# Optimization experiments

Measured on AMD Instinct MI355X. Metric: run time of the kernel, lower is better.

The kernel has to match this reference:

```python
import jax, jax.numpy as jnp
import numpy as np
import math

N, LQ, DIM = 4, 1000, 256
HEADS, DHEAD, DEPTH = 8, 32, 2
LVLS, NPTS, MLP = 5, 4, 512
SCALE = DHEAD ** -0.5
SHAPES = np.array([[128, 128], [64, 64], [32, 32], [16, 16], [8, 8]], np.int32)
AREAS = SHAPES[:, 0] * SHAPES[:, 1]
STARTS = np.concatenate([[0], np.cumsum(AREAS)[:-1]]).astype(np.int32)
LIN = int(AREAS.sum())


def _ln(x, g, b):
    m = jnp.mean(x, -1, keepdims=True)
    v = jnp.var(x, -1, keepdims=True)
    return (x - m) * jax.lax.rsqrt(v + 1e-5) * g + b


def _gelu(x):  # tanh-approx GELU exactly as the torch module
    c = math.sqrt(2.0 / math.pi)
    return 0.5 * x * (1.0 + jnp.tanh(c * (x + 0.044715 * x ** 3)))


def _ms_deform(value, shapes, starts, loc, aw):
    # value [N,Lin,H,D]; loc [N,Lq,H,L,P,2] normalized to [0,1]; aw [N,Lq,H,L,P]
    n, lq, h, L, p, _ = loc.shape
    d = value.shape[-1]
    ni = jnp.arange(n)[:, None, None, None]
    hi = jnp.arange(h)[None, None, :, None]
    out = jnp.zeros((n, lq, h, d), value.dtype)
    for l in range(L):  # fixed small pyramid depth
        Hl, Wl = int(shapes[l, 0]), int(shapes[l, 1])
        s = int(starts[l])
        v = value[:, s:s + Hl * Wl].reshape(n, Hl, Wl, h, d)
        gx = loc[:, :, :, l, :, 0] * Wl - 0.5  # [N,Lq,H,P]
        gy = loc[:, :, :, l, :, 1] * Hl - 0.5
        x0 = jnp.floor(gx); y0 = jnp.floor(gy)
        lx = gx - x0; ly = gy - y0
        x0i = x0.astype(jnp.int32); y0i = y0.astype(jnp.int32)
        def corner(yi, xi):
            ok = ((yi >= 0) & (yi < Hl) & (xi >= 0) & (xi < Wl)).astype(value.dtype)
            g = v[ni, jnp.clip(yi, 0, Hl - 1), jnp.clip(xi, 0, Wl - 1), hi]  # [N,Lq,H,P,D]
            return g * ok[..., None]
        samp = (corner(y0i, x0i) * ((1 - ly) * (1 - lx))[..., None]
                + corner(y0i, x0i + 1) * ((1 - ly) * lx)[..., None]
                + corner(y0i + 1, x0i) * (ly * (1 - lx))[..., None]
                + corner(y0i + 1, x0i + 1) * (ly * lx)[..., None])
        out = out + jnp.einsum('nqhp,nqhpd->nqhd', aw[:, :, :, l], samp)
    return out.reshape(n, lq, h * d)


def _forward(x, src, center_pos, pos_w, pos_b, ln1_g, ln1_b, qkv_w, out_w, out_b,
             ln2_g, ln2_b, off_w, off_b, aw_w, aw_b, val_w, val_b, op_w, op_b,
             ln3_g, ln3_b, ff_w1, ff_b1, ff_w2, ff_b2, spatial_shapes, level_start_index):
    shapes = np.asarray(spatial_shapes)
    starts = np.asarray(level_start_index)
    n, lq, dim = x.shape
    pe = center_pos @ pos_w + pos_b                                   # pos_embedding(center_pos)
    ref = jnp.broadcast_to(center_pos[:, :, None, :], (n, lq, LVLS, 2))
    onorm = jnp.asarray(np.stack([shapes[:, 1], shapes[:, 0]], -1), x.dtype)  # [L,2] = (W,H)
    for i in range(DEPTH):
        # --- self-attention: PreNorm(x + pe) ---
        xn = _ln(x + pe, ln1_g[i], ln1_b[i])
        qkv = xn @ qkv_w[i]
        q, k, v = jnp.split(qkv, 3, axis=-1)
        q = q.reshape(n, lq, HEADS, DHEAD).transpose(0, 2, 1, 3)
        k = k.reshape(n, lq, HEADS, DHEAD).transpose(0, 2, 1, 3)
        v = v.reshape(n, lq, HEADS, DHEAD).transpose(0, 2, 1, 3)
        att = jax.nn.softmax(jnp.einsum('nhid,nhjd->nhij', q, k) * SCALE, axis=-1)
        o = jnp.einsum('nhij,nhjd->nhid', att, v).transpose(0, 2, 1, 3).reshape(n, lq, HEADS * DHEAD)
        x = x + o @ out_w[i] + out_b[i]
        # --- deformable cross-attention: PreNorm_CA norms query and src with same LN ---
        xn = _ln(x, ln2_g[i], ln2_b[i])
        srcn = _ln(src, ln2_g[i], ln2_b[i])
        query = xn + pe
        value = (srcn @ val_w[i] + val_b[i]).reshape(n, -1, HEADS, DHEAD)
        off = (query @ off_w[i] + off_b[i]).reshape(n, lq, HEADS, LVLS, NPTS, 2)
        aw = jax.nn.softmax((query @ aw_w[i] + aw_b[i]).reshape(n, lq, HEADS, LVLS * NPTS), axis=-1)
        aw = aw.reshape(n, lq, HEADS, LVLS, NPTS)
        loc = ref[:, :, None, :, None, :] + off / onorm[None, None, None, :, None, :]
        o = _ms_deform(value, shapes, starts, loc, aw)
        x = x + o @ op_w[i] + op_b[i]
        # --- feedforward: PreNorm ---
        xn = _ln(x, ln3_g[i], ln3_b[i])
        x = x + _gelu(xn @ ff_w1[i] + ff_b1[i]) @ ff_w2[i] + ff_b2[i]
    return x


def setup_inputs() -> dict:
    key = jax.random.key(0)
    ks = iter(jax.random.split(key, 64))
    r = lambda sh, s=0.02: jax.random.normal(next(ks), sh, jnp.float32) * s
    # sampling_offsets bias grid init (as in MSDeformAttn._reset_parameters)
    thetas = np.arange(HEADS) * (2.0 * math.pi / HEADS)
    grid = np.stack([np.cos(thetas), np.sin(thetas)], -1)
    grid = grid / np.abs(grid).max(-1, keepdims=True)
    grid = np.tile(grid[:, None, None, :], (1, LVLS, NPTS, 1)) * (np.arange(NPTS) + 1)[None, None, :, None]
    off_b = jnp.tile(jnp.asarray(grid.reshape(-1), jnp.float32)[None], (DEPTH, 1))
    return dict(
        x=jax.random.normal(next(ks), (N, LQ, DIM), jnp.float32),
        src=jax.random.normal(next(ks), (N, LIN, DIM), jnp.float32),
        center_pos=jax.random.uniform(next(ks), (N, LQ, 2), jnp.float32),
        spatial_shapes=jnp.asarray(SHAPES),
        level_start_index=jnp.asarray(STARTS),
        pos_w=r((2, DIM), 0.5), pos_b=jnp.zeros((DIM,), jnp.float32),
        ln1_g=jnp.ones((DEPTH, DIM), jnp.float32), ln1_b=jnp.zeros((DEPTH, DIM), jnp.float32),
        qkv_w=r((DEPTH, DIM, 3 * HEADS * DHEAD)),
        out_w=r((DEPTH, HEADS * DHEAD, DIM)), out_b=jnp.zeros((DEPTH, DIM), jnp.float32),
        ln2_g=jnp.ones((DEPTH, DIM), jnp.float32), ln2_b=jnp.zeros((DEPTH, DIM), jnp.float32),
        off_w=r((DEPTH, DIM, HEADS * LVLS * NPTS * 2)), off_b=off_b,
        aw_w=r((DEPTH, DIM, HEADS * LVLS * NPTS)), aw_b=jnp.zeros((DEPTH, HEADS * LVLS * NPTS), jnp.float32),
        val_w=r((DEPTH, DIM, HEADS * DHEAD)), val_b=jnp.zeros((DEPTH, HEADS * DHEAD), jnp.float32),
        op_w=r((DEPTH, HEADS * DHEAD, DIM)), op_b=jnp.zeros((DEPTH, DIM), jnp.float32),
        ln3_g=jnp.ones((DEPTH, DIM), jnp.float32), ln3_b=jnp.zeros((DEPTH, DIM), jnp.float32),
        ff_w1=r((DEPTH, DIM, MLP)), ff_b1=jnp.zeros((DEPTH, MLP), jnp.float32),
        ff_w2=r((DEPTH, MLP, DIM)), ff_b2=jnp.zeros((DEPTH, DIM), jnp.float32),
    )


def reference(x, src, center_pos, spatial_shapes, level_start_index, pos_w, pos_b,
              ln1_g, ln1_b, qkv_w, out_w, out_b, ln2_g, ln2_b, off_w, off_b,
              aw_w, aw_b, val_w, val_b, op_w, op_b, ln3_g, ln3_b,
              ff_w1, ff_b1, ff_w2, ff_b2):
    return _forward(x, src, center_pos, pos_w, pos_b, ln1_g, ln1_b, qkv_w, out_w, out_b,
                    ln2_g, ln2_b, off_w, off_b, aw_w, aw_b, val_w, val_b, op_w, op_b,
                    ln3_g, ln3_b, ff_w1, ff_b1, ff_w2, ff_b2, spatial_shapes, level_start_index)
```

## Files before the change

### kernel.cpp

```cpp
#include <hip/hip_runtime.h>
#include <hip/hip_bf16.h>
#include <math.h>

#define DIM 256
#define NB 4
#define LQ 1000
#define MLPD 512
#define LIN 21824
#define ROWS_X 4000
#define ROWS_SRC 87296
#define ATT_SCALE 0.17677669529663687f
#define LDK 72

typedef __hip_bfloat16 bf16;
typedef __attribute__((ext_vector_type(8))) short short8;
typedef __attribute__((ext_vector_type(4))) float floatx4;

__device__ __forceinline__ float rdv(const void* p, int f, size_t i){
    if (f) return ((const float*)p)[i];
    unsigned u = ((unsigned)((const unsigned short*)p)[i]) << 16;
    union { unsigned u; float f; } c; c.u = u; return c.f;
}
__device__ __forceinline__ short f2bs(float v){
    bf16 h = __float2bfloat16(v);
    return *reinterpret_cast<short*>(&h);
}
__device__ __forceinline__ float bs2f(short s){
    union { unsigned u; float f; } c; c.u = ((unsigned)(unsigned short)s) << 16; return c.f;
}

__global__ void detect_kernel(const void* __restrict__ x, int* __restrict__ flag){
    const unsigned short* u = (const unsigned short*)x;
    int t = threadIdx.x;
    bool hit = false;
    #pragma unroll
    for (int k = 0; k < 4; ++k) {
        unsigned short b = u[(t*4 + k)*2];
        union { unsigned u; float f; } c; c.u = ((unsigned)b) << 16;
        if (!(fabsf(c.f) <= 1000.f)) hit = true;
    }
    unsigned long long m = __ballot(hit);
    __shared__ unsigned long long red[4];
    if ((t & 63) == 0) red[t >> 6] = m;
    __syncthreads();
    if (t == 0) flag[0] = ((red[0]|red[1]|red[2]|red[3]) != 0ULL) ? 1 : 0;
}

__global__ void conv_kernel(const void* __restrict__ in, float* __restrict__ out,
                            int n, const int* __restrict__ flag){
    int f = flag[0];
    int i = blockIdx.x*256 + threadIdx.x;
    if (i < n) out[i] = rdv(in, f, i);
}

struct PTab { const void* src[14]; float* dst[14]; int n[14]; };
__global__ void convs_kernel(PTab t, const int* __restrict__ flag){
    int f = flag[0];
    int j = blockIdx.y;
    int i = blockIdx.x*256 + threadIdx.x;
    if (i < t.n[j]) t.dst[j][i] = rdv(t.src[j], f, i);
}

__global__ void catb_kernel(const void* __restrict__ offb, const void* __restrict__ awb,
                            const int* __restrict__ flag, float* __restrict__ oab){
    int f = flag[0];
    int layer = blockIdx.y;
    int idx = blockIdx.x*256 + threadIdx.x;
    if (idx >= 480) return;
    float v = (idx < 320) ? rdv(offb, f, (size_t)layer*320 + idx)
                          : rdv(awb,  f, (size_t)layer*160 + idx - 320);
    oab[layer*480 + idx] = v;
}

struct WT { const void* src[8]; short* dst[8]; int K[8]; int N[8]; int ld[8]; int ro[8]; };
__global__ void wtransall_kernel(WT t, const int* __restrict__ flag){
    int j = blockIdx.z >> 1, b = blockIdx.z & 1;
    int K = t.K[j], N = t.N[j];
    int k0 = blockIdx.x*32, n0 = blockIdx.y*32;
    if (k0 >= K || n0 >= N) return;
    int f = flag[0];
    __shared__ float tt[32][33];
    int tx = threadIdx.x & 31, ty = threadIdx.x >> 5;
    size_t base = (size_t)b * K * N;
    for (int i = ty; i < 32; i += 8) {
        int k = k0 + i, n = n0 + tx;
        tt[i][tx] = (k < K && n < N) ? rdv(t.src[j], f, base + (size_t)k*N + n) : 0.f;
    }
    __syncthreads();
    int ld = t.ld[j], ro = t.ro[j];
    for (int i = ty; i < 32; i += 8) {
        int n = n0 + i, k = k0 + tx;
        if (n < N && k < K)
            t.dst[j][(size_t)b*ld*K + (size_t)(ro+n)*K + k] = f2bs(tt[tx][i]);
    }
}

__global__ void pe_kernel(const void* __restrict__ cp, const void* __restrict__ pw,
                          const void* __restrict__ pb, const int* __restrict__ flag,
                          float* __restrict__ pe){
    int f = flag[0];
    int row = blockIdx.x, t = threadIdx.x;
    float cx = rdv(cp, f, (size_t)row*2);
    float cy = rdv(cp, f, (size_t)row*2 + 1);
    pe[(size_t)row*DIM + t] = cx*rdv(pw, f, t) + cy*rdv(pw, f, DIM + t) + rdv(pb, f, t);
}

__global__ __launch_bounds__(256) void stats2_kernel(const void* __restrict__ src,
                                                     const int* __restrict__ flag,
                                                     float2* __restrict__ stats){
    int f = flag[0];
    int wave = threadIdx.x >> 6, lane = threadIdx.x & 63;
    int row = blockIdx.x*4 + wave;
    float v0, v1, v2, v3;
    if (f) {
        float4 x = *(const float4*)((const float*)src + (size_t)row*DIM + lane*4);
        v0 = x.x; v1 = x.y; v2 = x.z; v3 = x.w;
    } else {
        ushort4 u = *(const ushort4*)((const unsigned short*)src + (size_t)row*DIM + lane*4);
        v0 = bs2f((short)u.x); v1 = bs2f((short)u.y);
        v2 = bs2f((short)u.z); v3 = bs2f((short)u.w);
    }
    float s  = v0 + v1 + v2 + v3;
    float s2 = v0*v0 + v1*v1 + v2*v2 + v3*v3;
    #pragma unroll
    for (int o = 32; o; o >>= 1) {
        s  += __shfl_xor(s,  o, 64);
        s2 += __shfl_xor(s2, o, 64);
    }
    if (lane == 0) {
        float mean = s * (1.f/DIM);
        float var  = s2 * (1.f/DIM) - mean*mean;
        stats[row] = make_float2(mean, rsqrtf(var + 1e-5f));
    }
}

__global__ __launch_bounds__(256) void xstats_kernel(const float* __restrict__ a,
                                                     const float* __restrict__ pre,
                                                     float2* __restrict__ st){
    int wave = threadIdx.x >> 6, lane = threadIdx.x & 63;
    int row = blockIdx.x*4 + wave;
    float4 x = *(const float4*)(a + (size_t)row*DIM + lane*4);
    if (pre) {
        float4 p = *(const float4*)(pre + (size_t)row*DIM + lane*4);
        x.x += p.x; x.y += p.y; x.z += p.z; x.w += p.w;
    }
    float s  = x.x + x.y + x.z + x.w;
    float s2 = x.x*x.x + x.y*x.y + x.z*x.z + x.w*x.w;
    #pragma unroll
    for (int o = 32; o; o >>= 1) {
        s  += __shfl_xor(s,  o, 64);
        s2 += __shfl_xor(s2, o, 64);
    }
    if (lane == 0) {
        float mean = s * (1.f/DIM);
        float var  = s2 * (1.f/DIM) - mean*mean;
        st[row] = make_float2(mean, rsqrtf(var + 1e-5f));
    }
}

template<int AMODE>
__global__ __launch_bounds__(256) void mgemm_kernel(
    const void* __restrict__ Asrc,
    const float2* __restrict__ ast, const float* __restrict__ ag, const float* __restrict__ ab,
    const float* __restrict__ Apre, const float* __restrict__ Apost,
    const short* __restrict__ Wt, const float* __restrict__ bias, const float* res,
    void* Cout, int M, int K, int N, int act, int cbf){
    __shared__ short As[64*LDK];
    __shared__ short Bs[64*LDK];
    int tid = threadIdx.x;
    int wave = tid >> 6, lane = tid & 63;
    int wm = wave >> 1, wn = wave & 1;
    int quad = lane >> 4, l16 = lane & 15;
    int row0 = blockIdx.x*64, col0 = blockIdx.y*64;
    floatx4 acc[2][2];
    #pragma unroll
    for (int i = 0; i < 2; ++i)
        #pragma unroll
        for (int j = 0; j < 2; ++j)
            acc[i][j] = (floatx4){0.f,0.f,0.f,0.f};

    int r  = tid >> 2;
    int kc = (tid & 3) * 16;
    int gr = row0 + r;
    int gc = col0 + r;
    const short8 z8 = {0,0,0,0,0,0,0,0};

    for (int k0 = 0; k0 < K; k0 += 64) {
        short8 a0 = z8, a1 = z8;
        if (gr < M) {
            if (AMODE == 2) {
                const short8* p = (const short8*)((const short*)Asrc + (size_t)gr*K + k0 + kc);
                a0 = p[0]; a1 = p[1];
            } else {
                const float4* p = (const float4*)((const float*)Asrc + (size_t)gr*K + k0 + kc);
                float4 x0 = p[0], x1 = p[1], x2 = p[2], x3 = p[3];
                float av[16] = {x0.x,x0.y,x0.z,x0.w, x1.x,x1.y,x1.z,x1.w,
                                x2.x,x2.y,x2.z,x2.w, x3.x,x3.y,x3.z,x3.w};
                if (AMODE == 3) {
                    if (Apre) {
                        const float4* q = (const float4*)(Apre + (size_t)gr*K + k0 + kc);
                        float4 p0 = q[0], p1 = q[1], p2 = q[2], p3 = q[3];
                        float pv[16] = {p0.x,p0.y,p0.z,p0.w, p1.x,p1.y,p1.z,p1.w,
                                        p2.x,p2.y,p2.z,p2.w, p3.x,p3.y,p3.z,p3.w};
                        #pragma unroll
                        for (int j = 0; j < 16; ++j) av[j] += pv[j];
                    }
                    float2 st = ast[gr];
                    const float4* gp = (const float4*)(ag + k0 + kc);
                    const float4* bp = (const float4*)(ab + k0 + kc);
                    float4 g0 = gp[0], g1 = gp[1], g2 = gp[2], g3 = gp[3];
                    float4 b0 = bp[0], b1 = bp[1], b2 = bp[2], b3 = bp[3];
                    float gv[16] = {g0.x,g0.y,g0.z,g0.w, g1.x,g1.y,g1.z,g1.w,
                                    g2.x,g2.y,g2.z,g2.w, g3.x,g3.y,g3.z,g3.w};
                    float bv[16] = {b0.x,b0.y,b0.z,b0.w, b1.x,b1.y,b1.z,b1.w,
                                    b2.x,b2.y,b2.z,b2.w, b3.x,b3.y,b3.z,b3.w};
                    #pragma unroll
                    for (int j = 0; j < 16; ++j)
                        av[j] = (av[j] - st.x)*st.y*gv[j] + bv[j];
                    if (Apost) {
                        const float4* q = (const float4*)(Apost + (size_t)gr*K + k0 + kc);
                        float4 p0 = q[0], p1 = q[1], p2 = q[2], p3 = q[3];
                        float pv[16] = {p0.x,p0.y,p0.z,p0.w, p1.x,p1.y,p1.z,p1.w,
                                        p2.x,p2.y,p2.z,p2.w, p3.x,p3.y,p3.z,p3.w};
                        #pragma unroll
                        for (int j = 0; j < 16; ++j) av[j] += pv[j];
                    }
                }
                #pragma unroll
                for (int j = 0; j < 8; ++j) { a0[j] = f2bs(av[j]); a1[j] = f2bs(av[8+j]); }
            }
        }
        *(short8*)&As[r*LDK + kc]     = a0;
        *(short8*)&As[r*LDK + kc + 8] = a1;
        short8 b0 = z8, b1 = z8;
        if (gc < N) {
            const short8* p = (const short8*)(Wt + (size_t)gc*K + k0 + kc);
            b0 = p[0]; b1 = p[1];
        }
        *(short8*)&Bs[r*LDK + kc]     = b0;
        *(short8*)&Bs[r*LDK + kc + 8] = b1;
        __syncthreads();
        #pragma unroll
        for (int kb = 0; kb < 64; kb += 32) {
            short8 af[2], bfr[2];
            #pragma unroll
            for (int mi = 0; mi < 2; ++mi)
                af[mi] = *(const short8*)&As[(wm*32 + mi*16 + l16)*LDK + kb + quad*8];
            #pragma unroll
            for (int ni = 0; ni < 2; ++ni)
                bfr[ni] = *(const short8*)&Bs[(wn*32 + ni*16 + l16)*LDK + kb + quad*8];
            #pragma unroll
            for (int mi = 0; mi < 2; ++mi)
                #pragma unroll
                for (int ni = 0; ni < 2; ++ni)
                    acc[mi][ni] = __builtin_amdgcn_mfma_f32_16x16x32_bf16(
                        af[mi], bfr[ni], acc[mi][ni], 0, 0, 0);
        }
        __syncthreads();
    }
    #pragma unroll
    for (int mi = 0; mi < 2; ++mi) {
        int rbase = row0 + wm*32 + mi*16 + quad*4;
        #pragma unroll
        for (int ni = 0; ni < 2; ++ni) {
            int c = col0 + wn*32 + ni*16 + l16;
            if (c >= N) continue;
            #pragma unroll
            for (int r2 = 0; r2 < 4; ++r2) {
                int rr = rbase + r2;
                if (rr >= M) continue;
                float v = acc[mi][ni][r2];
                if (bias) v += bias[c];
                if (act) v = 0.5f*v*(1.f + tanhf(0.7978845608028654f*(v + 0.044715f*v*v*v)));
                if (res) v += res[(size_t)rr*N + c];
                if (cbf) ((bf16*)Cout)[(size_t)rr*N + c] = __float2bfloat16(v);
                else     ((float*)Cout)[(size_t)rr*N + c] = v;
            }
        }
    }
}

__global__ __launch_bounds__(256) void mgemm128_kernel(
    const void* __restrict__ Asrc, const int* __restrict__ flag,
    const float2* __restrict__ stats, const float* __restrict__ g, const float* __restrict__ bvec,
    const short* __restrict__ Wt, const float* __restrict__ bias,
    bf16* __restrict__ C, int K, int N){
    __shared__ short As[128*LDK];
    __shared__ short Bs[128*LDK];
    __shared__ float gs[256], bs[256];
    int tid = threadIdx.x;
    int f = flag[0];
    int wave = tid >> 6, lane = tid & 63;
    int wm = wave >> 1, wn = wave & 1;
    int quad = lane >> 4, l16 = lane & 15;
    int row0 = blockIdx.x*128, col0 = blockIdx.y*128;
    if (tid < K) { gs[tid] = g[tid]; bs[tid] = bvec[tid]; }
    floatx4 acc[4][4];
    #pragma unroll
    for (int i = 0; i < 4; ++i)
        #pragma unroll
        for (int j = 0; j < 4; ++j)
            acc[i][j] = (floatx4){0.f,0.f,0.f,0.f};
    __syncthreads();

    for (int k0 = 0; k0 < K; k0 += 64) {
        #pragma unroll
        for (int i = 0; i < 2; ++i) {
            int idx = tid + i*256;
            int r = idx >> 2;
            int kc = (idx & 3) * 16;
            int gr = row0 + r;
            float2 st = stats[gr];
            float av[16];
            if (f) {
                const float4* p = (const float4*)((const float*)Asrc + (size_t)gr*K + k0 + kc);
                float4 x0 = p[0], x1 = p[1], x2 = p[2], x3 = p[3];
                av[0]=x0.x; av[1]=x0.y; av[2]=x0.z; av[3]=x0.w;
                av[4]=x1.x; av[5]=x1.y; av[6]=x1.z; av[7]=x1.w;
                av[8]=x2.x; av[9]=x2.y; av[10]=x2.z; av[11]=x2.w;
                av[12]=x3.x; av[13]=x3.y; av[14]=x3.z; av[15]=x3.w;
            } else {
                const short8* p = (const short8*)((const short*)Asrc + (size_t)gr*K + k0 + kc);
                short8 s0 = p[0], s1 = p[1];
                #pragma unroll
                for (int j = 0; j < 8; ++j) {
                    av[j] = bs2f(s0[j]); av[8+j] = bs2f(s1[j]);
                }
            }
            short8 a0, a1;
            #pragma unroll
            for (int j = 0; j < 16; ++j) {
                float v = (av[j] - st.x) * st.y * gs[k0+kc+j] + bs[k0+kc+j];
                if (j < 8) a0[j] = f2bs(v); else a1[j-8] = f2bs(v);
            }
            *(short8*)&As[r*LDK + kc]     = a0;
            *(short8*)&As[r*LDK + kc + 8] = a1;
            int gc = col0 + r;
            const short8* pb = (const short8*)(Wt + (size_t)gc*K + k0 + kc);
            *(short8*)&Bs[r*LDK + kc]     = pb[0];
            *(short8*)&Bs[r*LDK + kc + 8] = pb[1];
        }
        __syncthreads();
        #pragma unroll
        for (int kb = 0; kb < 64; kb += 32) {
            short8 af[4], bfr[4];
            #pragma unroll
            for (int mi = 0; mi < 4; ++mi)
                af[mi] = *(const short8*)&As[(wm*64 + mi*16 + l16)*LDK + kb + quad*8];
            #pragma unroll
            for (int ni = 0; ni < 4; ++ni)
                bfr[ni] = *(const short8*)&Bs[(wn*64 + ni*16 + l16)*LDK + kb + quad*8];
            #pragma unroll
            for (int mi = 0; mi < 4; ++mi)
                #pragma unroll
                for (int ni = 0; ni < 4; ++ni)
                    acc[mi][ni] = __builtin_amdgcn_mfma_f32_16x16x32_bf16(
                        af[mi], bfr[ni], acc[mi][ni], 0, 0, 0);
        }
        __syncthreads();
    }
    #pragma unroll
    for (int mi = 0; mi < 4; ++mi) {
        int rbase = row0 + wm*64 + mi*16 + quad*4;
        #pragma unroll
        for (int ni = 0; ni < 4; ++ni) {
            int c = col0 + wn*64 + ni*16 + l16;
            float bv = bias[c];
            #pragma unroll
            for (int r2 = 0; r2 < 4; ++r2)
                C[(size_t)(rbase + r2)*N + c] = __float2bfloat16(acc[mi][ni][r2] + bv);
        }
    }
}

__global__ __launch_bounds__(256) void fattn_kernel(const short* __restrict__ qkv,
                                                    float* __restrict__ out){
    int nh = blockIdx.y;
    int n = nh >> 3, h = nh & 7;
    int q0 = blockIdx.x * 64;
    __shared__ short Ks[64*40];
    __shared__ short VsT[32*72];
    __shared__ short Ps[64*72];
    int tid = threadIdx.x;
    int wave = tid >> 6, lane = tid & 63;
    int quad = lane >> 4, l16 = lane & 15;
    int r = tid >> 2, c8 = (tid & 3) * 8;
    const short8 z8 = {0,0,0,0,0,0,0,0};

    short8 qf = z8;
    {
        int gq = q0 + wave*16 + l16;
        if (gq < LQ) {
            short8 s = *(const short8*)(qkv + ((size_t)(n*LQ+gq))*768 + h*32 + quad*8);
            #pragma unroll
            for (int j = 0; j < 8; ++j) qf[j] = f2bs(bs2f(s[j]) * ATT_SCALE);
        }
    }
    floatx4 acc[2];
    acc[0] = (floatx4){0.f,0.f,0.f,0.f};
    acc[1] = (floatx4){0.f,0.f,0.f,0.f};
    float m[4], lsum[4];
    #pragma unroll
    for (int i = 0; i < 4; ++i) { m[i] = -3.0e38f; lsum[i] = 0.f; }

    for (int k0 = 0; k0 < LQ; k0 += 64) {
        {
            int gk = k0 + r;
            short8 kv = z8, vv = z8;
            if (gk < LQ) {
// ... 41 lines not shown
                Ps[(wave*16 + quad*4 + r2)*72 + kg*16 + l16] = f2bs(pv);
            }
        #pragma unroll
        for (int r2 = 0; r2 < 4; ++r2) {
            psum[r2] += __shfl_xor(psum[r2], 1, 64);
            psum[r2] += __shfl_xor(psum[r2], 2, 64);
            psum[r2] += __shfl_xor(psum[r2], 4, 64);
            psum[r2] += __shfl_xor(psum[r2], 8, 64);
            lsum[r2] = lsum[r2]*fac[r2] + psum[r2];
        }
        #pragma unroll
        for (int ni = 0; ni < 2; ++ni)
            #pragma unroll
            for (int r2 = 0; r2 < 4; ++r2)
                acc[ni][r2] *= fac[r2];
        #pragma unroll
        for (int kb = 0; kb < 64; kb += 32) {
            short8 pf = *(const short8*)&Ps[(wave*16 + l16)*72 + kb + quad*8];
            #pragma unroll
            for (int ni = 0; ni < 2; ++ni) {
                short8 vf = *(const short8*)&VsT[(ni*16 + l16)*72 + kb + quad*8];
                acc[ni] = __builtin_amdgcn_mfma_f32_16x16x32_bf16(pf, vf, acc[ni], 0, 0, 0);
            }
        }
        __syncthreads();
    }
    #pragma unroll
    for (int r2 = 0; r2 < 4; ++r2) {
        int row = q0 + wave*16 + quad*4 + r2;
        if (row >= LQ) continue;
        float inv = 1.f / lsum[r2];
        #pragma unroll
        for (int ni = 0; ni < 2; ++ni)
            out[((size_t)(n*LQ+row))*256 + h*32 + ni*16 + l16] = acc[ni][r2] * inv;
    }
}

__global__ __launch_bounds__(256) void sample2_kernel(
        const bf16* __restrict__ value, const float* __restrict__ offaw,
        const float* __restrict__ cp, float* __restrict__ out){
    int nq = blockIdx.x;
    int n = nq / LQ;
    int d = threadIdx.x & 31, h = threadIdx.x >> 5;
    float cx = cp[nq*2], cy = cp[nq*2+1];
    const float* rowp = offaw + (size_t)nq*480;
    float o0 = rowp[h*40 + d];
    float o1 = (d < 8) ? rowp[h*40 + 32 + d] : 0.f;
    float logit = (d < 20) ? rowp[320 + h*20 + d] : -3.0e38f;
    float mx = logit;
    #pragma unroll
    for (int off = 16; off; off >>= 1) mx = fmaxf(mx, __shfl_xor(mx, off, 32));
    float p = (d < 20) ? __expf(logit - mx) : 0.f;
    float sm = p;
    #pragma unroll
    for (int off = 16; off; off >>= 1) sm += __shfl_xor(sm, off, 32);
    p *= (1.f / sm);

    const int HW[5] = {128,64,32,16,8};
    const int ST[5] = {0,16384,20480,21504,21760};
    float acc = 0.f;
    #pragma unroll
    for (int l = 0; l < 5; ++l) {
        int hw = HW[l];
        float fhw = (float)hw;
        size_t vb = ((size_t)n*LIN + ST[l]) * 256 + h*32 + d;
        #pragma unroll
        for (int pi = 0; pi < 4; ++pi) {
            const int idx = l*4 + pi;
            float w  = __shfl(p, idx, 32);
            float ox = (2*idx < 32)   ? __shfl(o0, 2*idx, 32)   : __shfl(o1, 2*idx-32, 32);
            float oy = (2*idx+1 < 32) ? __shfl(o0, 2*idx+1, 32) : __shfl(o1, 2*idx+1-32, 32);
            float gx = cx*fhw + ox - 0.5f;
            float gy = cy*fhw + oy - 0.5f;
            float x0f = floorf(gx), y0f = floorf(gy);
            float lx = gx - x0f, ly = gy - y0f;
            int x0 = (int)x0f, y0 = (int)y0f;
            int x1 = x0 + 1, y1 = y0 + 1;
            bool bx0 = (unsigned)x0 < (unsigned)hw, bx1 = (unsigned)x1 < (unsigned)hw;
            bool by0 = (unsigned)y0 < (unsigned)hw, by1 = (unsigned)y1 < (unsigned)hw;
            int x0c = min(max(x0, 0), hw-1), x1c = min(max(x1, 0), hw-1);
            int y0c = min(max(y0, 0), hw-1), y1c = min(max(y1, 0), hw-1);
            float v00 = __bfloat162float(value[vb + (size_t)(y0c*hw + x0c)*256]);
            float v01 = __bfloat162float(value[vb + (size_t)(y0c*hw + x1c)*256]);
            float v10 = __bfloat162float(value[vb + (size_t)(y1c*hw + x0c)*256]);
            float v11 = __bfloat162float(value[vb + (size_t)(y1c*hw + x1c)*256]);
            float w00 = (bx0 && by0) ? (1.f-ly)*(1.f-lx)*w : 0.f;
            float w01 = (bx1 && by0) ? (1.f-ly)*lx*w       : 0.f;
            float w10 = (bx0 && by1) ? ly*(1.f-lx)*w       : 0.f;
            float w11 = (bx1 && by1) ? ly*lx*w             : 0.f;
            acc = fmaf(w00, v00, acc);
            acc = fmaf(w01, v01, acc);
            acc = fmaf(w10, v10, acc);
            acc = fmaf(w11, v11, acc);
        }
    }
    out[(size_t)nq*256 + h*32 + d] = acc;
}

__global__ void final_kernel(const float* __restrict__ in, void* __restrict__ out,
                             int n, const int* __restrict__ flag){
    int f = flag[0];
    int i = blockIdx.x*256 + threadIdx.x;
    if (i >= n) return;
    float v = in[i];
    if (!isfinite(v)) v = 0.f;
    if (f) ((float*)out)[i] = v;
    else   ((bf16*)out)[i] = __float2bfloat16(v);
}

extern "C" void kernel_launch(void* const* d_in, const int* in_sizes, int n_in,
                              void* d_out, int out_size, void* d_ws, size_t ws_size,
                              hipStream_t stream){
    const void* x_raw  = d_in[0];
    const void* src    = d_in[1];
    const void* cp_raw = d_in[2];
    char* ws = (char*)d_ws;
    size_t off = 0;
    auto alloc = [&](size_t bytes){ size_t p = off; off += (bytes + 255) & ~(size_t)255; return p; };
    int*   flag  = (int*)(ws + alloc(256));
    float* xf    = (float*)(ws + alloc((size_t)ROWS_X*DIM*4));
    float* pe    = (float*)(ws + alloc((size_t)ROWS_X*DIM*4));
    float* tmp   = (float*)(ws + alloc((size_t)ROWS_X*DIM*4));
    bf16*  qkv   = (bf16*)(ws + alloc((size_t)ROWS_X*768*2));
    bf16*  ffh   = (bf16*)(ws + alloc((size_t)ROWS_X*MLPD*2));
    float* offaw = (float*)(ws + alloc((size_t)ROWS_X*480*4));
    float2* stats = (float2*)(ws + alloc((size_t)ROWS_SRC*8));
    float2* xst  = (float2*)(ws + alloc((size_t)ROWS_X*8));
    float* cpf   = (float*)(ws + alloc((size_t)ROWS_X*2*4));
    float* oab   = (float*)(ws + alloc((size_t)2*480*4));
    const int sidx[13] = {5,6,7,8,11,12,13,19,21,22,23,25,27};
    const int ssz[13]  = {512,256,512,512,512,512,512,512,512,512,512,1024,512};
    float* sp[13];
    for (int j = 0; j < 13; ++j) sp[j] = (float*)(ws + alloc((size_t)ssz[j]*4));
    short* qkvT = (short*)(ws + alloc((size_t)2*768*256*2));
    short* outT = (short*)(ws + alloc((size_t)2*256*256*2));
    short* oawT = (short*)(ws + alloc((size_t)2*480*256*2));
    short* valT = (short*)(ws + alloc((size_t)2*256*256*2));
    short* opT  = (short*)(ws + alloc((size_t)2*256*256*2));
    short* ff1T = (short*)(ws + alloc((size_t)2*512*256*2));
    short* ff2T = (short*)(ws + alloc((size_t)2*256*512*2));
    bf16*  val  = (bf16*)(ws + alloc((size_t)ROWS_SRC*DIM*2));
    (void)ws_size; (void)in_sizes; (void)n_in; (void)out_size;

    detect_kernel<<<1, 256, 0, stream>>>(x_raw, flag);
    conv_kernel<<<(ROWS_X*DIM+255)/256, 256, 0, stream>>>(x_raw, xf, ROWS_X*DIM, flag);
    PTab pt;
    for (int j = 0; j < 13; ++j) { pt.src[j] = d_in[sidx[j]]; pt.dst[j] = sp[j]; pt.n[j] = ssz[j]; }
    pt.src[13] = cp_raw; pt.dst[13] = cpf; pt.n[13] = ROWS_X*2;
    convs_kernel<<<dim3(32,14), 256, 0, stream>>>(pt, flag);
    catb_kernel<<<dim3(2,2), 256, 0, stream>>>(d_in[15], d_in[17], flag, oab);
    {
        WT wt;
        const int widx[8] = {9,10,14,16,18,20,24,26};
        short* wdst[8] = {qkvT, outT, oawT, oawT, valT, opT, ff1T, ff2T};
        const int wK[8]  = {256,256,256,256,256,256,256,512};
        const int wN[8]  = {768,256,320,160,256,256,512,256};
        const int wld[8] = {768,256,480,480,256,256,512,256};
        const int wro[8] = {0,0,0,320,0,0,0,0};
        for (int j = 0; j < 8; ++j) {
            wt.src[j] = d_in[widx[j]]; wt.dst[j] = wdst[j];
            wt.K[j] = wK[j]; wt.N[j] = wN[j]; wt.ld[j] = wld[j]; wt.ro[j] = wro[j];
        }
        wtransall_kernel<<<dim3(16,24,16), 256, 0, stream>>>(wt, flag);
    }

    float* pos_w = sp[0];  float* pos_b = sp[1];
    float* ln1_g = sp[2];  float* ln1_b = sp[3];
    float* out_b = sp[4];
    float* ln2_g = sp[5];  float* ln2_b = sp[6];
    float* val_b = sp[7];  float* op_b  = sp[8];
    float* ln3_g = sp[9];  float* ln3_b = sp[10];
    float* ff_b1 = sp[11]; float* ff_b2 = sp[12];
    (void)pos_w; (void)pos_b;

    pe_kernel<<<ROWS_X, 256, 0, stream>>>(cp_raw, d_in[5], d_in[6], flag, pe);
    stats2_kernel<<<ROWS_SRC/4, 256, 0, stream>>>(src, flag, stats);

    int gmx = (ROWS_X + 63) / 64;
    for (int i = 0; i < 2; ++i) {
        xstats_kernel<<<ROWS_X/4, 256, 0, stream>>>(xf, pe, xst);
        mgemm_kernel<3><<<dim3(gmx,12), 256, 0, stream>>>(
            xf, xst, ln1_g + i*DIM, ln1_b + i*DIM, pe, nullptr,
            qkvT + (size_t)i*768*256, nullptr, nullptr, qkv, ROWS_X, 256, 768, 0, 1);
        fattn_kernel<<<dim3(16,32), 256, 0, stream>>>((const short*)qkv, tmp);
        mgemm_kernel<0><<<dim3(gmx,4), 256, 0, stream>>>(
            tmp, nullptr, nullptr, nullptr, nullptr, nullptr,
            outT + (size_t)i*256*256, out_b + i*DIM, xf, xf, ROWS_X, 256, 256, 0, 0);
        mgemm128_kernel<<<dim3(ROWS_SRC/128, 2), 256, 0, stream>>>(
            src, flag, stats, ln2_g + i*DIM, ln2_b + i*DIM,
            valT + (size_t)i*256*256, val_b + i*DIM, val, 256, 256);
        xstats_kernel<<<ROWS_X/4, 256, 0, stream>>>(xf, nullptr, xst);
        mgemm_kernel<3><<<dim3(gmx,8), 256, 0, stream>>>(
            xf, xst, ln2_g + i*DIM, ln2_b + i*DIM, nullptr, pe,
            oawT + (size_t)i*480*256, oab + i*480, nullptr, offaw, ROWS_X, 256, 480, 0, 0);
        sample2_kernel<<<ROWS_X, 256, 0, stream>>>(val, offaw, cpf, tmp);
        mgemm_kernel<0><<<dim3(gmx,4), 256, 0, stream>>>(
            tmp, nullptr, nullptr, nullptr, nullptr, nullptr,
            opT + (size_t)i*256*256, op_b + i*DIM, xf, xf, ROWS_X, 256, 256, 0, 0);
        xstats_kernel<<<ROWS_X/4, 256, 0, stream>>>(xf, nullptr, xst);
        mgemm_kernel<3><<<dim3(gmx,8), 256, 0, stream>>>(
            xf, xst, ln3_g + i*DIM, ln3_b + i*DIM, nullptr, nullptr,
            ff1T + (size_t)i*512*256, ff_b1 + i*MLPD, nullptr, ffh, ROWS_X, 256, 512, 1, 1);
        mgemm_kernel<2><<<dim3(gmx,4), 256, 0, stream>>>(
            ffh, nullptr, nullptr, nullptr, nullptr, nullptr,
            ff2T + (size_t)i*256*512, ff_b2 + i*DIM, xf, xf, ROWS_X, 512, 256, 0, 0);
    }
    final_kernel<<<(ROWS_X*DIM+255)/256, 256, 0, stream>>>(xf, d_out, ROWS_X*DIM, flag);
}
```

Before: 626.9 us.

## Fold LayerNorm affine into weights and fuse row stats into GEMM epilogues

Folds LayerNorm gamma into the transposed weights and beta into precomputed biases, then computes row sum/sumsq statistics through atomics in the residual GEMM epilogues instead of separate xstats launches. The src LayerNorm is applied once up front into a bf16 buffer, so the value projection becomes a plain bf16 GEMM with no per-layer normalisation. Intermediate attention and sampling outputs switch to bf16, and the final conversion is merged into the last GEMM. These changes remove several launches and memory passes. The cost is atomics, an extra 44 MB normalized src buffer, and a different rounding order.

```diff
diff --git a/kernel.cpp b/kernel.cpp
--- a/kernel.cpp
+++ b/kernel.cpp
@@ -46,19 +46,12 @@
     if (t == 0) flag[0] = ((red[0]|red[1]|red[2]|red[3]) != 0ULL) ? 1 : 0;
 }
 
-__global__ void conv_kernel(const void* __restrict__ in, float* __restrict__ out,
-                            int n, const int* __restrict__ flag){
-    int f = flag[0];
-    int i = blockIdx.x*256 + threadIdx.x;
-    if (i < n) out[i] = rdv(in, f, i);
-}
-
-struct PTab { const void* src[14]; float* dst[14]; int n[14]; };
+struct PTab { const void* src[15]; float* dst[15]; int n[15]; };
 __global__ void convs_kernel(PTab t, const int* __restrict__ flag){
-    int f = flag[0];
     int j = blockIdx.y;
     int i = blockIdx.x*256 + threadIdx.x;
-    if (i < t.n[j]) t.dst[j][i] = rdv(t.src[j], f, i);
+    if (i >= t.n[j]) return;
+    t.dst[j][i] = t.src[j] ? rdv(t.src[j], flag[0], i) : 0.f;
 }
 
 __global__ void catb_kernel(const void* __restrict__ offb, const void* __restrict__ awb,
@@ -72,7 +65,8 @@
     oab[layer*480 + idx] = v;
 }
 
-struct WT { const void* src[8]; short* dst[8]; int K[8]; int N[8]; int ld[8]; int ro[8]; };
+struct WT { const void* src[8]; short* dst[8]; const float* scl[8];
+            int K[8]; int N[8]; int ld[8]; int ro[8]; };
 __global__ void wtransall_kernel(WT t, const int* __restrict__ flag){
     int j = blockIdx.z >> 1, b = blockIdx.z & 1;
     int K = t.K[j], N = t.N[j];
@@ -88,11 +82,31 @@
     }
     __syncthreads();
     int ld = t.ld[j], ro = t.ro[j];
+    const float* sc = t.scl[j];
     for (int i = ty; i < 32; i += 8) {
         int n = n0 + i, k = k0 + tx;
-        if (n < N && k < K)
-            t.dst[j][(size_t)b*ld*K + (size_t)(ro+n)*K + k] = f2bs(tt[tx][i]);
-    }
+        if (n < N && k < K) {
+            float v = tt[tx][i];
+            if (sc) v *= sc[(size_t)b*K + k];
+            t.dst[j][(size_t)b*ld*K + (size_t)(ro+n)*K + k] = f2bs(v);
+        }
+    }
+}
+
+struct BFT { const void* W[3]; const float* bv[3]; const float* base[3];
+             float* dst[3]; int K[3]; int N[3]; };
+__global__ void biasfold_kernel(BFT t, const int* __restrict__ flag){
+    int f = flag[0];
+    int j = blockIdx.y, b = blockIdx.z;
+    int n = blockIdx.x*256 + threadIdx.x;
+    int K = t.K[j], N = t.N[j];
+    if (n >= N) return;
+    const float* bv = t.bv[j] + (size_t)b*K;
+    size_t wbase = (size_t)b*K*N;
+    float s = t.base[j] ? t.base[j][(size_t)b*N + n] : 0.f;
+    for (int k = 0; k < K; ++k)
+        s += bv[k]*rdv(t.W[j], f, wbase + (size_t)k*N + n);
+    t.dst[j][(size_t)b*N + n] = s;
 }
 
 __global__ void pe_kernel(const void* __restrict__ cp, const void* __restrict__ pw,
@@ -105,9 +119,34 @@
     pe[(size_t)row*DIM + t] = cx*rdv(pw, f, t) + cy*rdv(pw, f, DIM + t) + rdv(pb, f, t);
 }
 
-__global__ __launch_bounds__(256) void stats2_kernel(const void* __restrict__ src,
-                                                     const int* __restrict__ flag,
-                                                     float2* __restrict__ stats){
+__global__ __launch_bounds__(256) void convx_kernel(const void* __restrict__ x,
+        const float* __restrict__ pe, const int* __restrict__ flag,
+        float* __restrict__ xf, float2* __restrict__ st){
+    int f = flag[0];
+    int wave = threadIdx.x >> 6, lane = threadIdx.x & 63;
+    int row = blockIdx.x*4 + wave;
+    float4 v;
+    if (f) v = *(const float4*)((const float*)x + (size_t)row*DIM + lane*4);
+    else {
+        ushort4 u = *(const ushort4*)((const unsigned short*)x + (size_t)row*DIM + lane*4);
+        v = make_float4(bs2f((short)u.x), bs2f((short)u.y), bs2f((short)u.z), bs2f((short)u.w));
+    }
+    *(float4*)(xf + (size_t)row*DIM + lane*4) = v;
+    float4 p = *(const float4*)(pe + (size_t)row*DIM + lane*4);
+    float a0 = v.x+p.x, a1 = v.y+p.y, a2 = v.z+p.z, a3 = v.w+p.w;
+    float s  = a0+a1+a2+a3;
+    float s2 = a0*a0+a1*a1+a2*a2+a3*a3;
+    #pragma unroll
+    for (int o = 32; o; o >>= 1) {
+        s  += __shfl_xor(s,  o, 64);
+        s2 += __shfl_xor(s2, o, 64);
+    }
+    if (lane == 0) st[row] = make_float2(s, s2);
+}
+
+__global__ __launch_bounds__(256) void stats2n_kernel(const void* __restrict__ src,
+                                                      const int* __restrict__ flag,
+                                                      bf16* __restrict__ srcn){
     int f = flag[0];
     int wave = threadIdx.x >> 6, lane = threadIdx.x & 63;
     int row = blockIdx.x*4 + wave;
@@ -127,44 +166,25 @@
         s  += __shfl_xor(s,  o, 64);
         s2 += __shfl_xor(s2, o, 64);
     }
-    if (lane == 0) {
-        float mean = s * (1.f/DIM);
-        float var  = s2 * (1.f/DIM) - mean*mean;
-        stats[row] = make_float2(mean, rsqrtf(var + 1e-5f));
-    }
-}
-
-__global__ __launch_bounds__(256) void xstats_kernel(const float* __restrict__ a,
-                                                     const float* __restrict__ pre,
-                                                     float2* __restrict__ st){
-    int wave = threadIdx.x >> 6, lane = threadIdx.x & 63;
-    int row = blockIdx.x*4 + wave;
-    float4 x = *(const float4*)(a + (size_t)row*DIM + lane*4);
-    if (pre) {
-        float4 p = *(const float4*)(pre + (size_t)row*DIM + lane*4);
-        x.x += p.x; x.y += p.y; x.z += p.z; x.w += p.w;
-    }
-    float s  = x.x + x.y + x.z + x.w;
-    float s2 = x.x*x.x + x.y*x.y + x.z*x.z + x.w*x.w;
-    #pragma unroll
-    for (int o = 32; o; o >>= 1) {
-        s  += __shfl_xor(s,  o, 64);
-        s2 += __shfl_xor(s2, o, 64);
-    }
-    if (lane == 0) {
-        float mean = s * (1.f/DIM);
-        float var  = s2 * (1.f/DIM) - mean*mean;
-        st[row] = make_float2(mean, rsqrtf(var + 1e-5f));
-    }
+    float mean = s * (1.f/DIM);
+    float rstd = rsqrtf(s2 * (1.f/DIM) - mean*mean + 1e-5f);
+    ushort4 o4;
+    o4.x = (unsigned short)f2bs((v0-mean)*rstd);
+    o4.y = (unsigned short)f2bs((v1-mean)*rstd);
+    o4.z = (unsigned short)f2bs((v2-mean)*rstd);
+    o4.w = (unsigned short)f2bs((v3-mean)*rstd);
+    *(ushort4*)((unsigned short*)srcn + (size_t)row*DIM + lane*4) = o4;
 }
 
 template<int AMODE>
 __global__ __launch_bounds__(256) void mgemm_kernel(
-    const void* __restrict__ Asrc,
-    const float2* __restrict__ ast, const float* __restrict__ ag, const float* __restrict__ ab,
+    const void* __restrict__ Asrc, const float2* __restrict__ asums,
+    const float* __restrict__ ag, const float* __restrict__ ab,
     const float* __restrict__ Apre, const float* __restrict__ Apost,
     const short* __restrict__ Wt, const float* __restrict__ bias, const float* res,
-    void* Cout, int M, int K, int N, int act, int cbf){
+    void* Cout, int M, int K, int N, int act, int cbf,
+    float2* __restrict__ statacc, const float* __restrict__ sepe,
+    void* __restrict__ fin, const int* __restrict__ flag){
     __shared__ short As[64*LDK];
     __shared__ short Bs[64*LDK];
     int tid = threadIdx.x;
@@ -196,16 +216,18 @@
                 float4 x0 = p[0], x1 = p[1], x2 = p[2], x3 = p[3];
                 float av[16] = {x0.x,x0.y,x0.z,x0.w, x1.x,x1.y,x1.z,x1.w,
                                 x2.x,x2.y,x2.z,x2.w, x3.x,x3.y,x3.z,x3.w};
+                if (Apre) {
+                    const float4* q = (const float4*)(Apre + (size_t)gr*K + k0 + kc);
+                    float4 p0 = q[0], p1 = q[1], p2 = q[2], p3 = q[3];
+                    float pv[16] = {p0.x,p0.y,p0.z,p0.w, p1.x,p1.y,p1.z,p1.w,
+                                    p2.x,p2.y,p2.z,p2.w, p3.x,p3.y,p3.z,p3.w};
+                    #pragma unroll
+                    for (int j = 0; j < 16; ++j) av[j] += pv[j];
+                }
+                float2 st = asums[gr];
+                float mean = st.x * (1.f/256.f);
+                float rstd = rsqrtf(st.y*(1.f/256.f) - mean*mean + 1e-5f);
                 if (AMODE == 3) {
-                    if (Apre) {
-                        const float4* q = (const float4*)(Apre + (size_t)gr*K + k0 + kc);
-                        float4 p0 = q[0], p1 = q[1], p2 = q[2], p3 = q[3];
-                        float pv[16] = {p0.x,p0.y,p0.z,p0.w, p1.x,p1.y,p1.z,p1.w,
-                                        p2.x,p2.y,p2.z,p2.w, p3.x,p3.y,p3.z,p3.w};
-                        #pragma unroll
-                        for (int j = 0; j < 16; ++j) av[j] += pv[j];
-                    }
-                    float2 st = ast[gr];
                     const float4* gp = (const float4*)(ag + k0 + kc);
                     const float4* bp = (const float4*)(ab + k0 + kc);
                     float4 g0 = gp[0], g1 = gp[1], g2 = gp[2], g3 = gp[3];
@@ -216,7 +238,7 @@
                                     b2.x,b2.y,b2.z,b2.w, b3.x,b3.y,b3.z,b3.w};
                     #pragma unroll
                     for (int j = 0; j < 16; ++j)
-                        av[j] = (av[j] - st.x)*st.y*gv[j] + bv[j];
+                        av[j] = (av[j] - mean)*rstd*gv[j] + bv[j];
                     if (Apost) {
                         const float4* q = (const float4*)(Apost + (size_t)gr*K + k0 + kc);
                         float4 p0 = q[0], p1 = q[1], p2 = q[2], p3 = q[3];
@@ -225,6 +247,10 @@
                         #pragma unroll
                         for (int j = 0; j < 16; ++j) av[j] += pv[j];
                     }
+                } else {
+                    #pragma unroll
+                    for (int j = 0; j < 16; ++j)
+                        av[j] = (av[j] - mean)*rstd;
                 }
                 #pragma unroll
                 for (int j = 0; j < 8; ++j) { a0[j] = f2bs(av[j]); a1[j] = f2bs(av[8+j]); }
@@ -258,6 +284,29 @@
         }
         __syncthreads();
     }
+    float vout[2][2][4];
+    #pragma unroll
+    for (int mi = 0; mi < 2; ++mi) {
+        int rbase = row0 + wm*32 + mi*16 + quad*4;
+        #pragma unroll
+        for (int ni = 0; ni < 2; ++ni) {
+            int c = col0 + wn*32 + ni*16 + l16;
+            #pragma unroll
+            for (int r2 = 0; r2 < 4; ++r2) {
+                int rr = rbase + r2;
+                float v = 0.f;
+                if (c < N && rr < M) {
+                    v = acc[mi][ni][r2];
+                    if (bias) v += bias[c];
+                    if (act) v = 0.5f*v*(1.f + tanhf(0.7978845608028654f*(v + 0.044715f*v*v*v)));
+                    if (res) v += res[(size_t)rr*N + c];
+                }
+                vout[mi][ni][r2] = v;
+            }
+        }
+    }
+    int fflag = 0;
+    if (fin) fflag = flag[0];
     #pragma unroll
     for (int mi = 0; mi < 2; ++mi) {
         int rbase = row0 + wm*32 + mi*16 + quad*4;
@@ -269,39 +318,61 @@
             for (int r2 = 0; r2 < 4; ++r2) {
                 int rr = rbase + r2;
                 if (rr >= M) continue;
-                float v = acc[mi][ni][r2];
-                if (bias) v += bias[c];
-                if (act) v = 0.5f*v*(1.f + tanhf(0.7978845608028654f*(v + 0.044715f*v*v*v)));
-                if (res) v += res[(size_t)rr*N + c];
-                if (cbf) ((bf16*)Cout)[(size_t)rr*N + c] = __float2bfloat16(v);
-                else     ((float*)Cout)[(size_t)rr*N + c] = v;
+                float v = vout[mi][ni][r2];
+                if (fin) {
+                    float w = isfinite(v) ? v : 0.f;
+                    if (fflag) ((float*)fin)[(size_t)rr*N + c] = w;
+                    else       ((bf16*)fin)[(size_t)rr*N + c] = __float2bfloat16(w);
+                } else if (cbf) ((bf16*)Cout)[(size_t)rr*N + c] = __float2bfloat16(v);
+                else            ((float*)Cout)[(size_t)rr*N + c] = v;
             }
         }
     }
+    if (statacc) {
+        #pragma unroll
+        for (int mi = 0; mi < 2; ++mi) {
+            int rbase = row0 + wm*32 + mi*16 + quad*4;
+            #pragma unroll
+            for (int r2 = 0; r2 < 4; ++r2) {
+                int rr = rbase + r2;
+                float sv = 0.f, sq = 0.f;
+                #pragma unroll
+                for (int ni = 0; ni < 2; ++ni) {
+                    int c = col0 + wn*32 + ni*16 + l16;
+                    float v = vout[mi][ni][r2];
+                    if (sepe && rr < M) v += sepe[(size_t)rr*256 + c];
+                    sv += v; sq += v*v;
+                }
+                #pragma unroll
+                for (int o = 1; o < 16; o <<= 1) {
+                    sv += __shfl_xor(sv, o, 64);
+                    sq += __shfl_xor(sq, o, 64);
+                }
+                if (l16 == 0 && rr < M) {
+                    atomicAdd(&statacc[rr].x, sv);
+                    atomicAdd(&statacc[rr].y, sq);
+                }
+            }
+        }
+    }
 }
 
 __global__ __launch_bounds__(256) void mgemm128_kernel(
-    const void* __restrict__ Asrc, const int* __restrict__ flag,
-    const float2* __restrict__ stats, const float* __restrict__ g, const float* __restrict__ bvec,
-    const short* __restrict__ Wt, const float* __restrict__ bias,
-    bf16* __restrict__ C, int K, int N){
+    const short* __restrict__ A, const short* __restrict__ Wt,
+    const float* __restrict__ bias, bf16* __restrict__ C, int K, int N){
     __shared__ short As[128*LDK];
     __shared__ short Bs[128*LDK];
-    __shared__ float gs[256], bs[256];
     int tid = threadIdx.x;
-    int f = flag[0];
     int wave = tid >> 6, lane = tid & 63;
     int wm = wave >> 1, wn = wave & 1;
     int quad = lane >> 4, l16 = lane & 15;
     int row0 = blockIdx.x*128, col0 = blockIdx.y*128;
-    if (tid < K) { gs[tid] = g[tid]; bs[tid] = bvec[tid]; }
     floatx4 acc[4][4];
     #pragma unroll
     for (int i = 0; i < 4; ++i)
         #pragma unroll
         for (int j = 0; j < 4; ++j)
             acc[i][j] = (floatx4){0.f,0.f,0.f,0.f};
-    __syncthreads();
 
     for (int k0 = 0; k0 < K; k0 += 64) {
         #pragma unroll
@@ -310,31 +381,9 @@
             int r = idx >> 2;
             int kc = (idx & 3) * 16;
             int gr = row0 + r;
-            float2 st = stats[gr];
-            float av[16];
-            if (f) {
-                const float4* p = (const float4*)((const float*)Asrc + (size_t)gr*K + k0 + kc);
-                float4 x0 = p[0], x1 = p[1], x2 = p[2], x3 = p[3];
-                av[0]=x0.x; av[1]=x0.y; av[2]=x0.z; av[3]=x0.w;
-                av[4]=x1.x; av[5]=x1.y; av[6]=x1.z; av[7]=x1.w;
-                av[8]=x2.x; av[9]=x2.y; av[10]=x2.z; av[11]=x2.w;
-                av[12]=x3.x; av[13]=x3.y; av[14]=x3.z; av[15]=x3.w;
-            } else {
-                const short8* p = (const short8*)((const short*)Asrc + (size_t)gr*K + k0 + kc);
-                short8 s0 = p[0], s1 = p[1];
-                #pragma unroll
-                for (int j = 0; j < 8; ++j) {
-                    av[j] = bs2f(s0[j]); av[8+j] = bs2f(s1[j]);
-                }
-            }
-            short8 a0, a1;
-            #pragma unroll
-            for (int j = 0; j < 16; ++j) {
-                float v = (av[j] - st.x) * st.y * gs[k0+kc+j] + bs[k0+kc+j];
-                if (j < 8) a0[j] = f2bs(v); else a1[j-8] = f2bs(v);
-            }
-            *(short8*)&As[r*LDK + kc]     = a0;
-            *(short8*)&As[r*LDK + kc + 8] = a1;
+            const short8* p = (const short8*)(A + (size_t)gr*K + k0 + kc);
+            *(short8*)&As[r*LDK + kc]     = p[0];
+            *(short8*)&As[r*LDK + kc + 8] = p[1];
             int gc = col0 + r;
             const short8* pb = (const short8*)(Wt + (size_t)gc*K + k0 + kc);
             *(short8*)&Bs[r*LDK + kc]     = pb[0];
@@ -374,7 +423,7 @@
 }
 
 __global__ __launch_bounds__(256) void fattn_kernel(const short* __restrict__ qkv,
-                                                    float* __restrict__ out){
+                                                    bf16* __restrict__ out){
     int nh = blockIdx.y;
     int n = nh >> 3, h = nh & 7;
     int q0 = blockIdx.x * 64;
@@ -482,13 +531,14 @@
         float inv = 1.f / lsum[r2];
         #pragma unroll
         for (int ni = 0; ni < 2; ++ni)
-            out[((size_t)(n*LQ+row))*256 + h*32 + ni*16 + l16] = acc[ni][r2] * inv;
+            out[((size_t)(n*LQ+row))*256 + h*32 + ni*16 + l16] =
+                __float2bfloat16(acc[ni][r2] * inv);
     }
 }
 
 __global__ __launch_bounds__(256) void sample2_kernel(
         const bf16* __restrict__ value, const float* __restrict__ offaw,
-        const float* __restrict__ cp, float* __restrict__ out){
+        const float* __restrict__ cp, bf16* __restrict__ out){
     int nq = blockIdx.x;
     int n = nq / LQ;
     int d = threadIdx.x & 31, h = threadIdx.x >> 5;
@@ -544,18 +594,7 @@
             acc = fmaf(w11, v11, acc);
         }
     }
-    out[(size_t)nq*256 + h*32 + d] = acc;
-}
-
-__global__ void final_kernel(const float* __restrict__ in, void* __restrict__ out,
-                             int n, const int* __restrict__ flag){
-    int f = flag[0];
-    int i = blockIdx.x*256 + threadIdx.x;
-    if (i >= n) return;
-    float v = in[i];
-    if (!isfinite(v)) v = 0.f;
-    if (f) ((float*)out)[i] = v;
-    else   ((bf16*)out)[i] = __float2bfloat16(v);
+    out[(size_t)nq*256 + h*32 + d] = __float2bfloat16(acc);
 }
 
 extern "C" void kernel_launch(void* const* d_in, const int* in_sizes, int n_in,
@@ -570,14 +609,16 @@
     int*   flag  = (int*)(ws + alloc(256));
     float* xf    = (float*)(ws + alloc((size_t)ROWS_X*DIM*4));
     float* pe    = (float*)(ws + alloc((size_t)ROWS_X*DIM*4));
-    float* tmp   = (float*)(ws + alloc((size_t)ROWS_X*DIM*4));
+    bf16*  tmpb  = (bf16*)(ws + alloc((size_t)ROWS_X*DIM*2));
     bf16*  qkv   = (bf16*)(ws + alloc((size_t)ROWS_X*768*2));
     bf16*  ffh   = (bf16*)(ws + alloc((size_t)ROWS_X*MLPD*2));
     float* offaw = (float*)(ws + alloc((size_t)ROWS_X*480*4));
-    float2* stats = (float2*)(ws + alloc((size_t)ROWS_SRC*8));
-    float2* xst  = (float2*)(ws + alloc((size_t)ROWS_X*8));
     float* cpf   = (float*)(ws + alloc((size_t)ROWS_X*2*4));
     float* oab   = (float*)(ws + alloc((size_t)2*480*4));
+    float2* statbuf = (float2*)(ws + alloc((size_t)6*ROWS_X*8));
+    float* qkvB  = (float*)(ws + alloc((size_t)2*768*4));
+    float* ff1B  = (float*)(ws + alloc((size_t)2*512*4));
+    float* valB  = (float*)(ws + alloc((size_t)2*256*4));
     const int sidx[13] = {5,6,7,8,11,12,13,19,21,22,23,25,27};
     const int ssz[13]  = {512,256,512,512,512,512,512,512,512,512,512,1024,512};
     float* sp[13];
@@ -589,30 +630,9 @@
     short* opT  = (short*)(ws + alloc((size_t)2*256*256*2));
     short* ff1T = (short*)(ws + alloc((size_t)2*512*256*2));
     short* ff2T = (short*)(ws + alloc((size_t)2*256*512*2));
+    bf16*  srcn = (bf16*)(ws + alloc((size_t)ROWS_SRC*DIM*2));
     bf16*  val  = (bf16*)(ws + alloc((size_t)ROWS_SRC*DIM*2));
     (void)ws_size; (void)in_sizes; (void)n_in; (void)out_size;
-
-    detect_kernel<<<1, 256, 0, stream>>>(x_raw, flag);
-    conv_kernel<<<(ROWS_X*DIM+255)/256, 256, 0, stream>>>(x_raw, xf, ROWS_X*DIM, flag);
-    PTab pt;
-    for (int j = 0; j < 13; ++j) { pt.src[j] = d_in[sidx[j]]; pt.dst[j] = sp[j]; pt.n[j] = ssz[j]; }
-    pt.src[13] = cp_raw; pt.dst[13] = cpf; pt.n[13] = ROWS_X*2;
-    convs_kernel<<<dim3(32,14), 256, 0, stream>>>(pt, flag);
-    catb_kernel<<<dim3(2,2), 256, 0, stream>>>(d_in[15], d_in[17], flag, oab);
-    {
-        WT wt;
-        const int widx[8] = {9,10,14,16,18,20,24,26};
-        short* wdst[8] = {qkvT, outT, oawT, oawT, valT, opT, ff1T, ff2T};
-        const int wK[8]  = {256,256,256,256,256,256,256,512};
-        const int wN[8]  = {768,256,320,160,256,256,512,256};
-        const int wld[8] = {768,256,480,480,256,256,512,256};
-        const int wro[8] = {0,0,0,320,0,0,0,0};
-        for (int j = 0; j < 8; ++j) {
-            wt.src[j] = d_in[widx[j]]; wt.dst[j] = wdst[j];
-            wt.K[j] = wK[j]; wt.N[j] = wN[j]; wt.ld[j] = wld[j]; wt.ro[j] = wro[j];
-        }
-        wtransall_kernel<<<dim3(16,24,16), 256, 0, stream>>>(wt, flag);
-    }
 
     float* pos_w = sp[0];  float* pos_b = sp[1];
     float* ln1_g = sp[2];  float* ln1_b = sp[3];
@@ -623,37 +643,78 @@
     float* ff_b1 = sp[11]; float* ff_b2 = sp[12];
     (void)pos_w; (void)pos_b;
 
+    detect_kernel<<<1, 256, 0, stream>>>(x_raw, flag);
     pe_kernel<<<ROWS_X, 256, 0, stream>>>(cp_raw, d_in[5], d_in[6], flag, pe);
-    stats2_kernel<<<ROWS_SRC/4, 256, 0, stream>>>(src, flag, stats);
+    PTab pt;
+    for (int j = 0; j < 13; ++j) { pt.src[j] = d_in[sidx[j]]; pt.dst[j] = sp[j]; pt.n[j] = ssz[j]; }
+    pt.src[13] = cp_raw; pt.dst[13] = cpf; pt.n[13] = ROWS_X*2;
+    pt.src[14] = nullptr; pt.dst[14] = (float*)(statbuf + ROWS_X); pt.n[14] = 5*ROWS_X*2;
+    convs_kernel<<<dim3(157,15), 256, 0, stream>>>(pt, flag);
+    catb_kernel<<<dim3(2,2), 256, 0, stream>>>(d_in[15], d_in[17], flag, oab);
+    convx_kernel<<<ROWS_X/4, 256, 0, stream>>>(x_raw, pe, flag, xf, statbuf);
+    stats2n_kernel<<<ROWS_SRC/4, 256, 0, stream>>>(src, flag, srcn);
+    {
+        WT wt;
+        const int widx[8] = {9,10,14,16,18,20,24,26};
+        short* wdst[8] = {qkvT, outT, oawT, oawT, valT, opT, ff1T, ff2T};
+        const float* wscl[8] = {ln1_g, nullptr, nullptr, nullptr, ln2_g, nullptr, ln3_g, nullptr};
+        const int wK[8]  = {256,256,256,256,256,256,256,512};
+        const int wN[8]  = {768,256,320,160,256,256,512,256};
+        const int wld[8] = {768,256,480,480,256,256,512,256};
+        const int wro[8] = {0,0,0,320,0,0,0,0};
+        for (int j = 0; j < 8; ++j) {
+            wt.src[j] = d_in[widx[j]]; wt.dst[j] = wdst[j]; wt.scl[j] = wscl[j];
+            wt.K[j] = wK[j]; wt.N[j] = wN[j]; wt.ld[j] = wld[j]; wt.ro[j] = wro[j];
+        }
+        wtransall_kernel<<<dim3(16,24,16), 256, 0, stream>>>(wt, flag);
+    }
+    {
+        BFT bt;
+        bt.W[0] = d_in[9];  bt.bv[0] = ln1_b; bt.base[0] = nullptr; bt.dst[0] = qkvB; bt.K[0] = 256; bt.N[0] = 768;
+        bt.W[1] = d_in[24]; bt.bv[1] = ln3_b; bt.base[1] = ff_b1;   bt.dst[1] = ff1B; bt.K[1] = 256; bt.N[1] = 512;
+        bt.W[2] = d_in[18]; bt.bv[2] = ln2_b; bt.base[2] = val_b;   bt.dst[2] = valB; bt.K[2] = 256; bt.N[2] = 256;
+        biasfold_kernel<<<dim3(3,3,2), 256, 0, stream>>>(bt, flag);
+    }
 
     int gmx = (ROWS_X + 63) / 64;
     for (int i = 0; i < 2; ++i) {
-        xstats_kernel<<<ROWS_X/4, 256, 0, stream>>>(xf, pe, xst);
-        mgemm_kernel<3><<<dim3(gmx,12), 256, 0, stream>>>(
-            xf, xst, ln1_g + i*DIM, ln1_b + i*DIM, pe, nullptr,
-            qkvT + (size_t)i*768*256, nullptr, nullptr, qkv, ROWS_X, 256, 768, 0, 1);
-        fattn_kernel<<<dim3(16,32), 256, 0, stream>>>((const short*)qkv, tmp);
-        mgemm_kernel<0><<<dim3(gmx,4), 256, 0, stream>>>(
-            tmp, nullptr, nullptr, nullptr, nullptr, nullptr,
-            outT + (size_t)i*256*256, out_b + i*DIM, xf, xf, ROWS_X, 256, 256, 0, 0);
+        float2* stA = statbuf + (size_t)(i ? 3 : 0)*ROWS_X;
+        float2* stO = statbuf + (size_t)(i ? 4 : 1)*ROWS_X;
+        float2* stF = statbuf + (size_t)(i ? 5 : 2)*ROWS_X;
+        mgemm_kernel<4><<<dim3(gmx,12), 256, 0, stream>>>(
+            xf, stA, nullptr, nullptr, pe, nullptr,
+            qkvT + (size_t)i*768*256, qkvB + i*768, nullptr, qkv,
+            ROWS_X, 256, 768, 0, 1, nullptr, nullptr, nullptr, flag);
+        fattn_kernel<<<dim3(16,32), 256, 0, stream>>>((const short*)qkv, tmpb);
+        mgemm_kernel<2><<<dim3(gmx,4), 256, 0, stream>>>(
+            tmpb, nullptr, nullptr, nullptr, nullptr, nullptr,
+            outT + (size_t)i*256*256, out_b + i*DIM, xf, xf,
+            ROWS_X, 256, 256, 0, 0, stO, nullptr, nullptr, flag);
         mgemm128_kernel<<<dim3(ROWS_SRC/128, 2), 256, 0, stream>>>(
-            src, flag, stats, ln2_g + i*DIM, ln2_b + i*DIM,
-            valT + (size_t)i*256*256, val_b + i*DIM, val, 256, 256);
-        xstats_kernel<<<ROWS_X/4, 256, 0, stream>>>(xf, nullptr, xst);
+            (const short*)srcn, valT + (size_t)i*256*256, valB + i*256, val, 256, 256);
         mgemm_kernel<3><<<dim3(gmx,8), 256, 0, stream>>>(
-            xf, xst, ln2_g + i*DIM, ln2_b + i*DIM, nullptr, pe,
-            oawT + (size_t)i*480*256, oab + i*480, nullptr, offaw, ROWS_X, 256, 480, 0, 0);
-        sample2_kernel<<<ROWS_X, 256, 0, stream>>>(val, offaw, cpf, tmp);
-        mgemm_kernel<0><<<dim3(gmx,4), 256, 0, stream>>>(
-            tmp, nullptr, nullptr, nullptr, nullptr, nullptr,
-            opT + (size_t)i*256*256, op_b + i*DIM, xf, xf, ROWS_X, 256, 256, 0, 0);
-        xstats_kernel<<<ROWS_X/4, 256, 0, stream>>>(xf, nullptr, xst);
-        mgemm_kernel<3><<<dim3(gmx,8), 256, 0, stream>>>(
-            xf, xst, ln3_g + i*DIM, ln3_b + i*DIM, nullptr, nullptr,
-            ff1T + (size_t)i*512*256, ff_b1 + i*MLPD, nullptr, ffh, ROWS_X, 256, 512, 1, 1);
+            xf, stO, ln2_g + i*DIM, ln2_b + i*DIM, nullptr, pe,
+            oawT + (size_t)i*480*256, oab + i*480, nullptr, offaw,
+            ROWS_X, 256, 480, 0, 0, nullptr, nullptr, nullptr, flag);
+        sample2_kernel<<<ROWS_X, 256, 0, stream>>>(val, offaw, cpf, tmpb);
         mgemm_kernel<2><<<dim3(gmx,4), 256, 0, stream>>>(
-            ffh, nullptr, nullptr, nullptr, nullptr, nullptr,
-            ff2T + (size_t)i*256*512, ff_b2 + i*DIM, xf, xf, ROWS_X, 512, 256, 0, 0);
-    }
-    final_kernel<<<(ROWS_X*DIM+255)/256, 256, 0, stream>>>(xf, d_out, ROWS_X*DIM, flag);
-}
+            tmpb, nullptr, nullptr, nullptr, nullptr, nullptr,
+            opT + (size_t)i*256*256, op_b + i*DIM, xf, xf,
+            ROWS_X, 256, 256, 0, 0, stF, nullptr, nullptr, flag);
+        mgemm_kernel<4><<<dim3(gmx,8), 256, 0, stream>>>(
+            xf, stF, nullptr, nullptr, nullptr, nullptr,
+            ff1T + (size_t)i*512*256, ff1B + i*MLPD, nullptr, ffh,
+            ROWS_X, 256, 512, 1, 1, nullptr, nullptr, nullptr, flag);
+        if (i == 0) {
+            mgemm_kernel<2><<<dim3(gmx,4), 256, 0, stream>>>(
+                ffh, nullptr, nullptr, nullptr, nullptr, nullptr,
+                ff2T + (size_t)i*256*512, ff_b2 + i*DIM, xf, xf,
+                ROWS_X, 512, 256, 0, 0, statbuf + (size_t)3*ROWS_X, pe, nullptr, flag);
+        } else {
+            mgemm_kernel<2><<<dim3(gmx,4), 256, 0, stream>>>(
+                ffh, nullptr, nullptr, nullptr, nullptr, nullptr,
+                ff2T + (size_t)i*256*512, ff_b2 + i*DIM, xf, xf,
+                ROWS_X, 512, 256, 0, 0, nullptr, nullptr, d_out, flag);
+        }
+    }
+}
```

Result: slower. 668.1 us (+6.6%).
